# Optimization experiments

Measured on AMD Instinct MI355X. Metric: run time of the kernel, lower is better.

## Reference

```python
import math
import jax, jax.numpy as jnp
import numpy as np

G_RATIO = 0.5
TB_FACTOR = 1e-3


def _expand(x):
    # x: [B,H,W]; 3x3 all-ones-except-center neighbor conv (same filter for every sample)
    k = jnp.ones((1, 1, 3, 3), x.dtype).at[0, 0, 1, 1].set(0.0)
    y = jax.lax.conv_general_dilated(x[:, None], k, (1, 1), 'SAME')
    return y[:, 0]


def _st_softmax_noexp(val):
    # straight-through normalized selection over flattened map
    B = val.shape[0]
    v = val.reshape(B, -1)
    y = v / v.sum(-1, keepdims=True)
    ind = jnp.argmax(y, -1)
    y_hard = jax.nn.one_hot(ind, y.shape[-1], dtype=y.dtype)
    y = y + jax.lax.stop_gradient(y_hard - y)
    return y.reshape(val.shape)


def _heuristic(gm):
    # gm: [B,H,W] one-hot goal maps -> Chebyshev + tb*Euclidean distance field
    B, H, W = gm.shape
    loc = jnp.stack(jnp.meshgrid(jnp.arange(H), jnp.arange(W), indexing='ij'), 0).astype(gm.dtype)  # [2,H,W]
    loc_e = loc.reshape(2, -1)[None]                      # [1,2,HW]
    goal_loc = jnp.einsum('kij,bij->bk', loc, gm)[:, :, None]  # [B,2,1]
    d = jnp.abs(loc_e - goal_loc)                         # [B,2,HW]
    h = d.sum(1) - d.min(1)
    euc = jnp.sqrt(((loc_e - goal_loc) ** 2).sum(1))
    return (h + TB_FACTOR * euc).reshape(B, H, W)


def _forward_core(cost_maps, start_maps, goal_maps, obstacles_maps):
    cm, sm, gm, om = cost_maps[:, 0], start_maps[:, 0], goal_maps[:, 0], obstacles_maps[:, 0]
    B, H, W = cm.shape
    h = _heuristic(gm) + cm
    goal_idx = jnp.argmax(gm.reshape(B, -1), -1)
    parents0 = jnp.broadcast_to(goal_idx[:, None].astype(cm.dtype), (B, H * W))
    inv_sqrt = 1.0 / math.sqrt(W)
    Tmax = W * W

    def step(carry, i):
        g, open_m, hist, parents, done, t = carry
        f = G_RATIO * g + (1.0 - G_RATIO) * h
        f_exp = jnp.exp(-f * inv_sqrt) * open_m
        snm = _st_softmax_noexp(f_exp)
        dist = (snm * gm).sum((1, 2), keepdims=True)
        unsolved = (dist < 1e-8).astype(cm.dtype)
        hist_n = jnp.clip(hist + snm, 0.0, 1.0)
        open_n = jnp.clip(open_m - unsolved * snm, 0.0, 1.0)
        nb = _expand(snm) * om
        g2 = _expand((g + cm) * snm)
        idx = ((1.0 - open_n) * (1.0 - hist_n) + open_n * (g > g2).astype(cm.dtype)) * nb
        idx = jax.lax.stop_gradient(idx)
        g_n = jax.lax.stop_gradient(g2 * idx + g * (1.0 - idx))
        open_n = jax.lax.stop_gradient(jnp.clip(open_n + idx, 0.0, 1.0))
        idx_f = idx.reshape(B, -1)
        new_par = jnp.argmax(snm.reshape(B, -1), -1)[:, None].astype(cm.dtype)
        par_n = new_par * idx_f + parents * (1.0 - idx_f)
        done_n = jnp.all(unsolved == 0)
        sel = lambda new, old: jnp.where(done, old, new)  # emulate the torch early break
        carry_n = (sel(g_n, g), sel(open_n, open_m), sel(hist_n, hist), sel(par_n, parents),
                   jnp.logical_or(done, done_n), jnp.where(done, t, i))
        return carry_n, None

    init = (jnp.zeros_like(sm), sm, jnp.zeros_like(sm), parents0,
            jnp.array(False), jnp.array(0, jnp.int32))
    (g, open_m, hist, parents, done, t), _ = jax.lax.scan(
        step, init, jnp.arange(Tmax, dtype=jnp.int32))
    return hist[:, None], parents, t


def _backtrack(goal_maps, parents, t):
    gm = goal_maps[:, 0]
    B, H, W = gm.shape
    par_i = parents.astype(jnp.int32)
    goal_f = gm.reshape(B, -1).astype(jnp.int32)
    loc = (par_i * goal_f).sum(-1)
    rng = jnp.arange(B)

    def bt(i, val):
        path, loc = val
        path = path.at[rng, loc].set(1)
        loc = jnp.take_along_axis(par_i, loc[:, None], -1)[:, 0]
        return (path, loc)

    path, _ = jax.lax.fori_loop(0, t, bt, (goal_f, loc))
    return path.reshape(B, 1, H, W)


def setup_inputs() -> dict:
    key = jax.random.key(0)
    k1, k2, k3, k4 = jax.random.split(key, 4)
    B, H, W = 16, 32, 32
    cost_maps = jax.random.uniform(k1, (B, 1, H, W), dtype=jnp.float32)
    sidx = jax.random.randint(k2, (B,), 0, H * W)
    gidx = jax.random.randint(k3, (B,), 0, H * W)
    gidx = jnp.where(gidx == sidx, (gidx + 1) % (H * W), gidx)
    start_maps = jax.nn.one_hot(sidx, H * W, dtype=jnp.float32).reshape(B, 1, H, W)
    goal_maps = jax.nn.one_hot(gidx, H * W, dtype=jnp.float32).reshape(B, 1, H, W)
    obstacles_maps = (jax.random.uniform(k4, (B, 1, H, W)) > 0.05).astype(jnp.float32)
    obstacles_maps = jnp.clip(obstacles_maps + start_maps + goal_maps, 0.0, 1.0)
    return {'cost_maps': cost_maps, 'start_maps': start_maps,
            'goal_maps': goal_maps, 'obstacles_maps': obstacles_maps}


def reference(cost_maps, start_maps, goal_maps, obstacles_maps):
    histories, parents, t = _forward_core(cost_maps, start_maps, goal_maps, obstacles_maps)
    path_maps = _backtrack(goal_maps, parents, t)
    return histories, path_maps
```

## Files before the change

kernel.cpp:

```cpp
#include <hip/hip_runtime.h>
#include <math.h>

#define HW 1024
#define NB 16
#define TMAXS 1024

typedef unsigned long long ull;

__device__ __forceinline__ double u2d(ull u) {
  return __longlong_as_double((long long)u);
}
__device__ __forceinline__ ull d2u(double d) {
  return (ull)__double_as_longlong(d);
}

__device__ __forceinline__ float keyhalf(float gh, float hh) {
#pragma clang fp contract(off)
  const float INV = 0.17677669529663687f;
  return expf(-(gh + hh) * INV);
}

template <int CTRL>
__device__ __forceinline__ double dpp_fmax64(double x) {
  ull u = d2u(x);
  int lo = (int)(unsigned)u;
  int hi = (int)(unsigned)(u >> 32);
  int lo2 = __builtin_amdgcn_update_dpp(0, lo, CTRL, 0xF, 0xF, false);
  int hi2 = __builtin_amdgcn_update_dpp(0, hi, CTRL, 0xF, 0xF, false);
  double y = u2d(((ull)(unsigned)hi2 << 32) | (unsigned)lo2);
  return fmax(x, y);
}

extern "C" __global__ void __launch_bounds__(64) astar_fused(
    const float* __restrict__ cm_g, const float* __restrict__ sm_g,
    const float* __restrict__ gm_g, const float* __restrict__ om_g,
    float* __restrict__ out) {
#pragma clang fp contract(off)
  const int b = blockIdx.x;
  const int lane = threadIdx.x;

  __shared__ __align__(16) ull key2[HW];
  __shared__ __align__(16) float4 gch[HW];
  __shared__ __align__(16) unsigned flg[HW];
  __shared__ __align__(16) unsigned par[HW];
  __shared__ __align__(16) ull level1[64];
  const float* gchf = (const float*)gch;

  const float* cm = cm_g + b * HW;
  const float* sm = sm_g + b * HW;
  const float* gm = gm_g + b * HW;
  const float* om = om_g + b * HW;

  float4 c4[4], o4[4];
  int gi = -1, si = -1;
#pragma unroll
  for (int q = 0; q < 4; ++q) {
    const int base = q * 256 + lane * 4;
    c4[q] = *(const float4*)(cm + base);
    o4[q] = *(const float4*)(om + base);
    const float4 s4 = *(const float4*)(sm + base);
    const float4 g4 = *(const float4*)(gm + base);
    const float sv[4] = {s4.x, s4.y, s4.z, s4.w};
    const float gv[4] = {g4.x, g4.y, g4.z, g4.w};
#pragma unroll
    for (int j = 0; j < 4; ++j) {
      if (gv[j] > 0.5f) gi = base + j;
      if (sv[j] > 0.5f) si = base + j;
    }
  }
#pragma unroll
  for (int m = 32; m >= 1; m >>= 1) {
    const int og = __shfl_xor(gi, m, 64);
    const int os = __shfl_xor(si, m, 64);
    gi = (og > gi) ? og : gi;
    si = (os > si) ? os : si;
  }
  const int goal = gi, start = si;

  level1[lane] = 0ull;
  const float grf = (float)(goal >> 5), gcf = (float)(goal & 31);
#pragma unroll
  for (int q = 0; q < 4; ++q) {
    const int base = q * 256 + lane * 4;
    const float cv[4] = {c4[q].x, c4[q].y, c4[q].z, c4[q].w};
    const float ov[4] = {o4[q].x, o4[q].y, o4[q].z, o4[q].w};
    ull pk[4];
    unsigned fv[4];
#pragma unroll
    for (int j = 0; j < 4; ++j) {
      const int cell = base + j;
      const float rr = (float)(cell >> 5), cc = (float)(cell & 31);
      const float dr = fabsf(rr - grf), dc = fabsf(cc - gcf);
      const float h0 = (dr + dc) - fminf(dr, dc);
      const float euc = sqrtf(dr * dr + dc * dc);
      const float t1 = 0.001f * euc;
      const float hh = h0 + t1;
      const float hf = hh + cv[j];
      const float hw = 0.5f * hf;
      gch[cell] = make_float4(0.0f, cv[j], 0.5f * cv[j], hw);
      fv[j] = (ov[j] > 0.5f) ? 1u : 0u;
      pk[j] = (ull)(1023 - cell);
      if (cell == start) {
        fv[j] |= 2u;
        pk[j] |= d2u((double)keyhalf(0.0f, hw));
      }
      atomicMax(&level1[cell >> 4], pk[j]);
    }
    *(uint4*)&flg[base] = make_uint4(fv[0], fv[1], fv[2], fv[3]);
    *(uint4*)&par[base] =
        make_uint4((unsigned)goal, (unsigned)goal, (unsigned)goal, (unsigned)goal);
    ulonglong2 k01, k23;
    k01.x = pk[0]; k01.y = pk[1];
    k23.x = pk[2]; k23.y = pk[3];
    *(ulonglong2*)&key2[base] = k01;
    *(ulonglong2*)&key2[base + 2] = k23;
  }
  __builtin_amdgcn_wave_barrier();
  ull stale = level1[lane];

  int dro = 0, dco = 0;
  if (lane < 8) {
    const int k = (lane < 4) ? lane : lane + 1;
    dro = k / 3 - 1;
    dco = k % 3 - 1;
  }

  int sel = start;
  bool reached = false;

#pragma unroll 1
  for (int step = 0; step < TMAXS; ++step) {
    if (sel == goal) { reached = true; break; }
    const int gp = sel >> 4;

    if (lane == 8) level1[gp] = 0ull;
    const float g2h = gchf[4 * sel + 2];
    int n = -1;
    if (lane < 8) {
      const int nr = (sel >> 5) + dro, nc = (sel & 31) + dco;
      if ((unsigned)nr < 32u && (unsigned)nc < 32u) n = (nr << 5) | nc;
    } else if (lane == 8) {
      n = sel;
    }
    unsigned f = 0;
    if (n >= 0) f = flg[n];
    float4 v = make_float4(0.f, 0.f, 0.f, 0.f);
    if (lane < 8 && n >= 0) v = gch[n];
    ull gc = 0ull;
    const bool grpLane = (lane >= 32) && (lane < 48);
    const int gcell = gp * 16 + (lane - 32);
    if (grpLane) {
      gc = key2[gcell];
      if (gcell == sel) gc = (ull)(1023 - sel);
    }

    double mp = (lane == gp) ? 0.0 : u2d(stale);
    mp = dpp_fmax64<0x111>(mp);
    mp = dpp_fmax64<0x112>(mp);
    mp = dpp_fmax64<0x114>(mp);
    mp = dpp_fmax64<0x118>(mp);
    mp = dpp_fmax64<0x142>(mp);
    mp = dpp_fmax64<0x143>(mp);
    const ull mpb = d2u(mp);
    const int mp_lo = __builtin_amdgcn_readlane((int)(unsigned)mpb, 63);
    const int mp_hi = __builtin_amdgcn_readlane((int)(unsigned)(mpb >> 32), 63);

    const float g2full = g2h + g2h;
    bool updv = false;
    ull pk = 0ull;
    if (lane < 8 && n >= 0) {
      updv = (f & 1u) && (((f & 6u) == 0u) || (((f & 2u) != 0u) && (v.x > g2full)));
      if (updv) pk = d2u((double)keyhalf(g2h, v.w)) | (ull)(1023 - n);
    }

    double ml = 0.0;
    if (grpLane) ml = u2d(gc);
    if (updv) ml = u2d(pk);
    ml = dpp_fmax64<0x111>(ml);
    ml = dpp_fmax64<0x112>(ml);
    ml = dpp_fmax64<0x114>(ml);
    ml = dpp_fmax64<0x118>(ml);
    const ull mlb = d2u(ml);
    const int a_lo = __builtin_amdgcn_readlane((int)(unsigned)mlb, 15);
    const int a_hi = __builtin_amdgcn_readlane((int)(unsigned)(mlb >> 32), 15);
    const int b_lo = __builtin_amdgcn_readlane((int)(unsigned)mlb, 47);
    const int b_hi = __builtin_amdgcn_readlane((int)(unsigned)(mlb >> 32), 47);

    const ull A  = ((ull)(unsigned)a_hi << 32) | (unsigned)a_lo;
    const ull B  = ((ull)(unsigned)b_hi << 32) | (unsigned)b_lo;
    const ull MP = ((ull)(unsigned)mp_hi << 32) | (unsigned)mp_lo;
    ull M = (A > B) ? A : B;
    M = (M > MP) ? M : MP;
    const int nsel = 1023 - (int)((unsigned)M & 1023u);

    if (grpLane) atomicMax(&level1[gp], gc);
    if (updv) {
      gch[n] = make_float4(g2full, v.y, 0.5f * (g2full + v.y), v.w);
      par[n] = (unsigned)sel;
    }
    if (updv || lane == 8) {
      flg[n] = (lane == 8) ? ((f | 4u) & ~2u) : (f | 2u);
      key2[n] = (lane == 8) ? (ull)(1023 - sel) : pk;
    }
    if (updv) atomicMax(&level1[n >> 4], pk);
    stale = level1[lane];

    sel = nsel;
    __builtin_amdgcn_wave_barrier();
  }
  if (reached && lane == 0) flg[goal] |= 4u;
  __builtin_amdgcn_wave_barrier();

  if (lane == 0) {
    const unsigned pv = par[goal];
    par[goal] = pv | 0x80000000u;
    unsigned loc = pv & 1023u;
#pragma unroll 1
    for (int i = 0; i < HW; ++i) {
      const unsigned w = par[loc];
      if (w & 0x80000000u) break;
      par[loc] = w | 0x80000000u;
      loc = w & 1023u;
    }
  }
  __builtin_amdgcn_wave_barrier();

#pragma unroll
  for (int q = 0; q < 4; ++q) {
    const int base = q * 256 + lane * 4;
    float4 hv, pv;
    hv.x = (flg[base + 0] & 4u) ? 1.0f : 0.0f;
    hv.y = (flg[base + 1] & 4u) ? 1.0f : 0.0f;
    hv.z = (flg[base + 2] & 4u) ? 1.0f : 0.0f;
    hv.w = (flg[base + 3] & 4u) ? 1.0f : 0.0f;
    pv.x = (par[base + 0] >> 31) ? 1.0f : 0.0f;
    pv.y = (par[base + 1] >> 31) ? 1.0f : 0.0f;
    pv.z = (par[base + 2] >> 31) ? 1.0f : 0.0f;
    pv.w = (par[base + 3] >> 31) ? 1.0f : 0.0f;
    *(float4*)(out + b * HW + base) = hv;
    *(float4*)(out + NB * HW + b * HW + base) = pv;
  }
}

extern "C" void kernel_launch(void* const* d_in, const int* in_sizes, int n_in,
                              void* d_out, int out_size, void* d_ws,
                              size_t ws_size, hipStream_t stream) {
  const float* cm = (const float*)d_in[0];
  const float* sm = (const float*)d_in[1];
  const float* gm = (const float*)d_in[2];
  const float* om = (const float*)d_in[3];
  float* out = (float*)d_out;
  hipLaunchKernelGGL(astar_fused, dim3(NB), dim3(64), 0, stream, cm, sm, gm,
                     om, out);
}
```

Measured before the change: 79.17 us.

## Pack per-cell state into skewed LDS records and shorten per-step reduction chain

Merges the separate g/cost/heuristic and flag arrays into one 16-byte record per cell, stored at a skewed LDS index so the eight neighbour reads fall in different banks. Each step now fetches a cell's state with a single vector load. The previous per-lane global max is folded into the group reduction, so the winner is read with one readlane of the low word instead of three 64-bit readlane pairs and scalar compares. Boundary handling becomes a precomputed neighbour mask and a flat offset. The key still stores g in halved form (g2h = 0.5*g2full), which could introduce small rounding differences versus the previous stored values.

```diff
diff --git a/kernel.cpp b/kernel.cpp
--- a/kernel.cpp
+++ b/kernel.cpp
@@ -31,6 +31,8 @@
   return fmax(x, y);
 }
 
+__device__ __forceinline__ int skew(int c) { return c + 3 * (c >> 5); }
+
 extern "C" __global__ void __launch_bounds__(64) astar_fused(
     const float* __restrict__ cm_g, const float* __restrict__ sm_g,
     const float* __restrict__ gm_g, const float* __restrict__ om_g,
@@ -39,12 +41,10 @@
   const int b = blockIdx.x;
   const int lane = threadIdx.x;
 
+  __shared__ __align__(16) uint4 cellT[1117];
   __shared__ __align__(16) ull key2[HW];
-  __shared__ __align__(16) float4 gch[HW];
-  __shared__ __align__(16) unsigned flg[HW];
   __shared__ __align__(16) unsigned par[HW];
   __shared__ __align__(16) ull level1[64];
-  const float* gchf = (const float*)gch;
 
   const float* cm = cm_g + b * HW;
   const float* sm = sm_g + b * HW;
@@ -75,7 +75,8 @@
     gi = (og > gi) ? og : gi;
     si = (os > si) ? os : si;
   }
-  const int goal = gi, start = si;
+  const int goal = __builtin_amdgcn_readfirstlane(gi);
+  const int start = __builtin_amdgcn_readfirstlane(si);
 
   level1[lane] = 0ull;
   const float grf = (float)(goal >> 5), gcf = (float)(goal & 31);
@@ -85,7 +86,6 @@
     const float cv[4] = {c4[q].x, c4[q].y, c4[q].z, c4[q].w};
     const float ov[4] = {o4[q].x, o4[q].y, o4[q].z, o4[q].w};
     ull pk[4];
-    unsigned fv[4];
 #pragma unroll
     for (int j = 0; j < 4; ++j) {
       const int cell = base + j;
@@ -97,16 +97,17 @@
       const float hh = h0 + t1;
       const float hf = hh + cv[j];
       const float hw = 0.5f * hf;
-      gch[cell] = make_float4(0.0f, cv[j], 0.5f * cv[j], hw);
-      fv[j] = (ov[j] > 0.5f) ? 1u : 0u;
+      unsigned fv = (ov[j] > 0.5f) ? 1u : 0u;
       pk[j] = (ull)(1023 - cell);
       if (cell == start) {
-        fv[j] |= 2u;
+        fv |= 2u;
         pk[j] |= d2u((double)keyhalf(0.0f, hw));
       }
+      cellT[skew(cell)] = make_uint4(__float_as_uint(0.0f),
+                                     __float_as_uint(cv[j]),
+                                     __float_as_uint(hw), fv);
       atomicMax(&level1[cell >> 4], pk[j]);
     }
-    *(uint4*)&flg[base] = make_uint4(fv[0], fv[1], fv[2], fv[3]);
     *(uint4*)&par[base] =
         make_uint4((unsigned)goal, (unsigned)goal, (unsigned)goal, (unsigned)goal);
     ulonglong2 k01, k23;
@@ -118,11 +119,10 @@
   __builtin_amdgcn_wave_barrier();
   ull stale = level1[lane];
 
-  int dro = 0, dco = 0;
-  if (lane < 8) {
+  int dlt = 0;
+  {
     const int k = (lane < 4) ? lane : lane + 1;
-    dro = k / 3 - 1;
-    dco = k % 3 - 1;
+    dlt = (k / 3 - 1) * 32 + (k % 3 - 1);
   }
 
   int sel = start;
@@ -132,27 +132,23 @@
   for (int step = 0; step < TMAXS; ++step) {
     if (sel == goal) { reached = true; break; }
     const int gp = sel >> 4;
-
-    if (lane == 8) level1[gp] = 0ull;
-    const float g2h = gchf[4 * sel + 2];
-    int n = -1;
-    if (lane < 8) {
-      const int nr = (sel >> 5) + dro, nc = (sel & 31) + dco;
-      if ((unsigned)nr < 32u && (unsigned)nc < 32u) n = (nr << 5) | nc;
-    } else if (lane == 8) {
-      n = sel;
-    }
-    unsigned f = 0;
-    if (n >= 0) f = flg[n];
-    float4 v = make_float4(0.f, 0.f, 0.f, 0.f);
-    if (lane < 8 && n >= 0) v = gch[n];
-    ull gc = 0ull;
-    const bool grpLane = (lane >= 32) && (lane < 48);
-    const int gcell = gp * 16 + (lane - 32);
-    if (grpLane) {
-      gc = key2[gcell];
-      if (gcell == sel) gc = (ull)(1023 - sel);
-    }
+    const int sxsel = skew(sel);
+
+    const int sr = sel >> 5, sc = sel & 31;
+    unsigned vmask = 0xFFu;
+    if (sr == 0) vmask &= ~0x07u;
+    if (sr == 31) vmask &= ~0xE0u;
+    if (sc == 0) vmask &= ~0x29u;
+    if (sc == 31) vmask &= ~0x94u;
+
+    if (lane == 16) level1[gp] = 0ull;
+    const uint4 sv = cellT[sxsel];
+    const int n = sel + dlt;
+    const bool relaxer = (lane < 8) && ((vmask >> lane) & 1u);
+    uint4 nv = make_uint4(0u, 0u, 0u, 0u);
+    if (relaxer) nv = cellT[skew(n)];
+    ull gco = 0ull;
+    if (lane < 16) gco = key2[gp * 16 + lane];
 
     double mp = (lane == gp) ? 0.0 : u2d(stale);
     mp = dpp_fmax64<0x111>(mp);
@@ -164,51 +160,54 @@
     const ull mpb = d2u(mp);
     const int mp_lo = __builtin_amdgcn_readlane((int)(unsigned)mpb, 63);
     const int mp_hi = __builtin_amdgcn_readlane((int)(unsigned)(mpb >> 32), 63);
-
-    const float g2full = g2h + g2h;
+    const double mpd = u2d(((ull)(unsigned)mp_hi << 32) | (unsigned)mp_lo);
+
+    const float g2full = __uint_as_float(sv.x) + __uint_as_float(sv.y);
+    const float g2h = 0.5f * g2full;
+    const unsigned f = nv.w;
     bool updv = false;
     ull pk = 0ull;
-    if (lane < 8 && n >= 0) {
-      updv = (f & 1u) && (((f & 6u) == 0u) || (((f & 2u) != 0u) && (v.x > g2full)));
-      if (updv) pk = d2u((double)keyhalf(g2h, v.w)) | (ull)(1023 - n);
-    }
+    if (relaxer) {
+      updv = (f & 1u) &&
+             (((f & 6u) == 0u) ||
+              (((f & 2u) != 0u) && (__uint_as_float(nv.x) > g2full)));
+      if (updv)
+        pk = d2u((double)keyhalf(g2h, __uint_as_float(nv.z))) | (ull)(1023 - n);
+    }
+    ull gcp = gco;
+    if (lane < 16 && (gp * 16 + lane) == sel) gcp = (ull)(1023 - sel);
+
+    const bool wr = updv || (lane == 8);
+    if (wr) {
+      uint4 wv;
+      wv.x = updv ? __float_as_uint(g2full) : sv.x;
+      wv.y = updv ? nv.y : sv.y;
+      wv.z = updv ? nv.z : sv.z;
+      wv.w = updv ? (f | 2u) : 5u;
+      cellT[updv ? skew(n) : sxsel] = wv;
+      key2[updv ? n : sel] = updv ? pk : (ull)(1023 - sel);
+    }
+    if (updv) par[n] = (unsigned)sel;
+    if (lane < 16) atomicMax(&level1[gp], gcp);
+    if (updv) atomicMax(&level1[n >> 4], pk);
+    const ull stale_n = level1[lane];
 
     double ml = 0.0;
-    if (grpLane) ml = u2d(gc);
-    if (updv) ml = u2d(pk);
+    if (lane < 16) ml = u2d(gcp);
+    if (updv) ml = fmax(ml, u2d(pk));
+    ml = fmax(ml, mpd);
     ml = dpp_fmax64<0x111>(ml);
     ml = dpp_fmax64<0x112>(ml);
     ml = dpp_fmax64<0x114>(ml);
     ml = dpp_fmax64<0x118>(ml);
-    const ull mlb = d2u(ml);
-    const int a_lo = __builtin_amdgcn_readlane((int)(unsigned)mlb, 15);
-    const int a_hi = __builtin_amdgcn_readlane((int)(unsigned)(mlb >> 32), 15);
-    const int b_lo = __builtin_amdgcn_readlane((int)(unsigned)mlb, 47);
-    const int b_hi = __builtin_amdgcn_readlane((int)(unsigned)(mlb >> 32), 47);
-
-    const ull A  = ((ull)(unsigned)a_hi << 32) | (unsigned)a_lo;
-    const ull B  = ((ull)(unsigned)b_hi << 32) | (unsigned)b_lo;
-    const ull MP = ((ull)(unsigned)mp_hi << 32) | (unsigned)mp_lo;
-    ull M = (A > B) ? A : B;
-    M = (M > MP) ? M : MP;
-    const int nsel = 1023 - (int)((unsigned)M & 1023u);
-
-    if (grpLane) atomicMax(&level1[gp], gc);
-    if (updv) {
-      gch[n] = make_float4(g2full, v.y, 0.5f * (g2full + v.y), v.w);
-      par[n] = (unsigned)sel;
-    }
-    if (updv || lane == 8) {
-      flg[n] = (lane == 8) ? ((f | 4u) & ~2u) : (f | 2u);
-      key2[n] = (lane == 8) ? (ull)(1023 - sel) : pk;
-    }
-    if (updv) atomicMax(&level1[n >> 4], pk);
-    stale = level1[lane];
-
-    sel = nsel;
+    const int lo15 = __builtin_amdgcn_readlane((int)(unsigned)d2u(ml), 15);
+    sel = 1023 - (lo15 & 1023);
+    stale = stale_n;
     __builtin_amdgcn_wave_barrier();
   }
-  if (reached && lane == 0) flg[goal] |= 4u;
+  if (reached && lane == 0) {
+    cellT[skew(goal)].w |= 4u;
+  }
   __builtin_amdgcn_wave_barrier();
 
   if (lane == 0) {
@@ -229,10 +228,10 @@
   for (int q = 0; q < 4; ++q) {
     const int base = q * 256 + lane * 4;
     float4 hv, pv;
-    hv.x = (flg[base + 0] & 4u) ? 1.0f : 0.0f;
-    hv.y = (flg[base + 1] & 4u) ? 1.0f : 0.0f;
-    hv.z = (flg[base + 2] & 4u) ? 1.0f : 0.0f;
-    hv.w = (flg[base + 3] & 4u) ? 1.0f : 0.0f;
+    hv.x = (cellT[skew(base + 0)].w & 4u) ? 1.0f : 0.0f;
+    hv.y = (cellT[skew(base + 1)].w & 4u) ? 1.0f : 0.0f;
+    hv.z = (cellT[skew(base + 2)].w & 4u) ? 1.0f : 0.0f;
+    hv.w = (cellT[skew(base + 3)].w & 4u) ? 1.0f : 0.0f;
     pv.x = (par[base + 0] >> 31) ? 1.0f : 0.0f;
     pv.y = (par[base + 1] >> 31) ? 1.0f : 0.0f;
     pv.z = (par[base + 2] >> 31) ? 1.0f : 0.0f;
```

New measurement: 98.79 us. 1.25x slower.
